# Performance work log

Measured on AMD Instinct MI355X. Metric: run time of the kernel, lower is better.

Reference implementation:

```python
import jax, jax.numpy as jnp
import numpy as np
from jax import lax

B, S, D = 8, 1024, 128

def setup_inputs() -> dict:
    key = jax.random.key(0)
    ks = jax.random.split(key, 6)
    scale = 1.0 / np.sqrt(D)
    return {
        "x": jax.random.normal(ks[0], (B, S, D), dtype=jnp.float32),
        "Wk": jax.random.normal(ks[1], (D, D), dtype=jnp.float32) * scale,
        "Wv": jax.random.normal(ks[2], (D, D), dtype=jnp.float32) * scale,
        "Wq": jax.random.normal(ks[3], (D, D), dtype=jnp.float32) * scale,
        "Wg": jax.random.normal(ks[4], (D, 3), dtype=jnp.float32) * scale,
        "bg": jnp.zeros((3,), dtype=jnp.float32),
    }

def reference(x, Wk, Wv, Wq, Wg, bg):
    b, s, d = x.shape
    k = x @ Wk  # [b,s,d]
    v = x @ Wv
    q = x @ Wq
    gates = jax.nn.sigmoid(x @ Wg + bg)  # [b,s,3]
    alpha, eta, theta = gates[..., 0], gates[..., 1], gates[..., 2]  # [b,s]

    M0 = jnp.zeros((b, d, d), dtype=x.dtype)
    S0 = jnp.zeros((b, d, d), dtype=x.dtype)

    # time-major scan inputs
    xs = (jnp.swapaxes(k, 0, 1), jnp.swapaxes(v, 0, 1), jnp.swapaxes(q, 0, 1),
          jnp.swapaxes(alpha, 0, 1), jnp.swapaxes(eta, 0, 1), jnp.swapaxes(theta, 0, 1))

    def scan_fn(carry, inp):
        M_prev, S_prev = carry
        kt, vt, qt, at, et, tt = inp  # kt/vt/qt: [b,d]; at/et/tt: [b]
        # NOTE: original einsum 'bd,bdd->bd' takes the DIAGONAL of M (faithful)
        diagM = jnp.einsum('bdd->bd', M_prev)  # [b,d]
        yt = qt * diagM
        pred = kt * diagM
        error = pred - vt
        grad = kt[:, :, None] * error[:, None, :]  # outer product [b,d,d]
        S_new = et[:, None, None] * S_prev - tt[:, None, None] * grad
        M_new = (1.0 - at[:, None, None]) * M_prev + S_new
        return (M_new, S_new), yt

    (M_final, S_final), outputs = lax.scan(scan_fn, (M0, S0), xs)
    outputs = jnp.swapaxes(outputs, 0, 1)  # [b,s,d]
    return (outputs, (M_final, S_final))
```

## Files before the change

### kernel.cpp

```cpp
#include <hip/hip_runtime.h>
#include <math.h>

#define NB 8
#define NS 1024
#define ND 128
#define NC 64
#define NL 16

#define OFF_K  0u
#define OFF_Q  1048576u
#define OFF_V  2097152u
#define OFF_E  3145728u
#define OFF_GA 4194304u
#define OFF_GE 4202496u
#define OFF_GT 4210688u
#define OFF_W  4218880u
#define OFF_C  4227072u
#define OFF_P  4235264u

#define PL_A00 (OFF_P)
#define PL_A01 (OFF_P +  65536u)
#define PL_A10 (OFF_P + 131072u)
#define PL_A11 (OFF_P + 196608u)
#define PL_B0  (OFF_P + 262144u)
#define PL_B1  (OFF_P + 327680u)
#define PL_MST (OFF_P + 393216u)
#define PL_SST (OFF_P + 458752u)
#define PL_WCA (OFF_P + 524288u)
#define PL_WCB (OFF_P + 524800u)
#define PL_WCD (OFF_P + 525312u)
#define PL_WRQ (OFF_P + 525824u)
#define PL_WRP (OFF_P + 526336u)
#define PL_WRA (OFF_P + 526848u)
#define OFF_WT (OFF_P + 532480u)
#define WT_LO  49152u

typedef short bf16x8 __attribute__((ext_vector_type(8)));
typedef float f32x4  __attribute__((ext_vector_type(4)));

static __device__ __forceinline__ unsigned short f2bf(float f) {
    unsigned u = __builtin_bit_cast(unsigned, f);
    unsigned r = (u + 0x7FFFu + ((u >> 16) & 1u)) >> 16;
    return (unsigned short)r;
}
static __device__ __forceinline__ float bf2f(unsigned short h) {
    unsigned u = ((unsigned)h) << 16;
    return __builtin_bit_cast(float, u);
}
static __device__ __forceinline__ unsigned pack2(float a, float b) {
    return (unsigned)f2bf(a) | ((unsigned)f2bf(b) << 16);
}
static __device__ __forceinline__ void split2(float a, float b,
                                              unsigned& hi, unsigned& lo) {
    unsigned short ah = f2bf(a), bh = f2bf(b);
    float ar = a - bf2f(ah), br = b - bf2f(bh);
    hi = (unsigned)ah | ((unsigned)bh << 16);
    lo = (unsigned)f2bf(ar) | ((unsigned)f2bf(br) << 16);
}

__global__ __launch_bounds__(256) void wtprep_kernel(
    const float* __restrict__ Wk, const float* __restrict__ Wv,
    const float* __restrict__ Wq, unsigned short* __restrict__ wtg)
{
    const int m    = blockIdx.x >> 4;
    const int cgrp = blockIdx.x & 15;
    const int tid  = threadIdx.x;
    const int cl   = tid >> 5;
    const int h    = tid & 31;
    const int c    = cgrp * 8 + cl;
    const float* W = (m == 0) ? Wk : (m == 1) ? Wv : Wq;

    float f[4];
#pragma unroll
    for (int i = 0; i < 4; ++i)
        f[i] = W[(h * 4 + i) * ND + c];
    uint2 hi, lo;
    split2(f[0], f[1], hi.x, lo.x);
    split2(f[2], f[3], hi.y, lo.y);
    const unsigned base = (unsigned)m * 16384u + (unsigned)c * 128u + (unsigned)h * 4u;
    *(uint2*)&wtg[base]         = hi;
    *(uint2*)&wtg[WT_LO + base] = lo;
}

__global__ __launch_bounds__(256) void proj_mfma(
    const float* __restrict__ x, const unsigned short* __restrict__ wtg,
    const float* __restrict__ Wg, const float* __restrict__ bg,
    float* __restrict__ Kb, float* __restrict__ Vb, float* __restrict__ Qb,
    float* __restrict__ ga, float* __restrict__ ge, float* __restrict__ gt)
{
    __shared__ unsigned short xs_hi[32 * 136];
    __shared__ unsigned short xs_lo[32 * 136];
    __shared__ unsigned short wt_hi[64 * 136];
    __shared__ unsigned short wt_lo[64 * 136];

    const int tid  = threadIdx.x;
    const int bid  = blockIdx.x;
    const int m    = bid >> 9;
    const int rt   = (bid >> 1) & 255;
    const int ch   = bid & 1;
    const int row0 = rt * 32;

    const float4* x4 = (const float4*)x;
#pragma unroll
    for (int l = 0; l < 4; ++l) {
        int idx = tid + l * 256;
        int r = idx >> 5, kq = idx & 31;
        float4 f = x4[(row0 + r) * 32 + kq];
        uint2 hi, lo;
        split2(f.x, f.y, hi.x, lo.x);
        split2(f.z, f.w, hi.y, lo.y);
        *(uint2*)&xs_hi[r * 136 + kq * 4] = hi;
        *(uint2*)&xs_lo[r * 136 + kq * 4] = lo;
    }
    const uint4* wh4 = (const uint4*)(wtg + m * 16384 + ch * 64 * 128);
    const uint4* wl4 = (const uint4*)(wtg + WT_LO + m * 16384 + ch * 64 * 128);
#pragma unroll
    for (int l = 0; l < 4; ++l) {
        int idx = tid + l * 256;
        int c = idx >> 4, u = idx & 15;
        *(uint4*)&wt_hi[c * 136 + u * 8] = wh4[c * 16 + u];
        *(uint4*)&wt_lo[c * 136 + u * 8] = wl4[c * 16 + u];
    }
    __syncthreads();

    const int wid  = tid >> 6;
    const int lane = tid & 63;
    const int rg   = wid >> 1;
    const int cg   = wid & 1;
    const int lrow = rg * 16 + (lane & 15);
    const int quad = lane >> 4;

    f32x4 acc[2];
    acc[0] = (f32x4){0.f, 0.f, 0.f, 0.f};
    acc[1] = (f32x4){0.f, 0.f, 0.f, 0.f};

#pragma unroll
    for (int kk = 0; kk < 4; ++kk) {
        bf16x8 ah = *(const bf16x8*)&xs_hi[lrow * 136 + kk * 32 + quad * 8];
        bf16x8 al = *(const bf16x8*)&xs_lo[lrow * 136 + kk * 32 + quad * 8];
#pragma unroll
        for (int ct = 0; ct < 2; ++ct) {
            int cl = cg * 32 + ct * 16 + (lane & 15);
            bf16x8 bh = *(const bf16x8*)&wt_hi[cl * 136 + kk * 32 + quad * 8];
            bf16x8 bl = *(const bf16x8*)&wt_lo[cl * 136 + kk * 32 + quad * 8];
            acc[ct] = __builtin_amdgcn_mfma_f32_16x16x32_bf16(ah, bh, acc[ct], 0, 0, 0);
            acc[ct] = __builtin_amdgcn_mfma_f32_16x16x32_bf16(ah, bl, acc[ct], 0, 0, 0);
            acc[ct] = __builtin_amdgcn_mfma_f32_16x16x32_bf16(al, bh, acc[ct], 0, 0, 0);
        }
    }

    float* dst = (m == 0) ? Kb : (m == 1) ? Vb : Qb;
#pragma unroll
    for (int ct = 0; ct < 2; ++ct) {
        int ocol = ch * 64 + cg * 32 + ct * 16 + (lane & 15);
#pragma unroll
        for (int r4 = 0; r4 < 4; ++r4) {
            int orow = row0 + rg * 16 + quad * 4 + r4;
            dst[orow * ND + ocol] = acc[ct][r4];
        }
    }

    if (m == 0 && ch == 0 && tid < 96) {
        int r = tid / 3, j = tid % 3;
        float z = bg[j];
        const float* xr = x + (row0 + r) * ND;
#pragma unroll 4
        for (int i = 0; i < ND; ++i)
            z = fmaf(xr[i], Wg[i * 3 + j], z);
        float gate = 1.0f / (1.0f + expf(-z));
        int row = row0 + r;
        float* gd = (j == 0) ? ga : (j == 1) ? ge : gt;
        gd[row] = gate;
    }
}

__global__ __launch_bounds__(128) void scan_phase1(
    const float* __restrict__ Kb, const float* __restrict__ Vb,
    const float* __restrict__ ga, const float* __restrict__ ge,
    const float* __restrict__ gt, float* __restrict__ ws)
{
    __shared__ float la[NL], le[NL], lt[NL];
    const int tid = threadIdx.x;
    const int b   = blockIdx.x >> 6;
    const int c   = blockIdx.x & 63;
    const int t0  = c * NL;
    const int g0  = b * NS + t0;

    if (tid < 16)       la[tid]      = ga[g0 + tid];
    else if (tid < 32)  le[tid - 16] = ge[g0 + tid - 16];
    else if (tid < 48)  lt[tid - 32] = gt[g0 + tid - 32];
    __syncthreads();

    const int d = tid;
    float A00 = 1.f, A01 = 0.f, A10 = 0.f, A11 = 1.f, B0 = 0.f, B1 = 0.f;
    int base = g0 * ND + d;
#pragma unroll
    for (int t = 0; t < NL; ++t) {
        float k = Kb[base], v = Vb[base];
        float a = la[t], e = le[t], th = lt[t];
        float tk = th * k;
        float gg = -tk * k;
        float h  = tk * v;
        float p  = (1.0f - a) + gg;
        float u0 = e * A10;
        float u1 = e * A11;
        float u2 = fmaf(e, B1, h);
        float n00 = fmaf(p, A00, u0), n10 = fmaf(gg, A00, u0);
        float n01 = fmaf(p, A01, u1), n11 = fmaf(gg, A01, u1);
        float nb0 = fmaf(p, B0, u2),  nb1 = fmaf(gg, B0, u2);
        A00 = n00; A01 = n01; A10 = n10; A11 = n11; B0 = nb0; B1 = nb1;
        base += ND;
    }
    const int pidx = (b * NC + c) * ND + d;
    ws[PL_A00 + pidx] = A00;
    ws[PL_A01 + pidx] = A01;
    ws[PL_A10 + pidx] = A10;
    ws[PL_A11 + pidx] = A11;
    ws[PL_B0  + pidx] = B0;
    ws[PL_B1  + pidx] = B1;

    if (tid == 0) {
        float al = 1.f, be = 1.f, de = 0.f;
#pragma unroll
        for (int t = NL - 1; t >= 0; --t) {
            float e1 = le[t];
            float o1 = 1.0f - la[t];
            de = fmaf(e1, de, o1 * be);
            al *= e1;
            be *= o1;
        }
        ws[PL_WCA + b * NC + c] = al;
        ws[PL_WCB + b * NC + c] = be;
        ws[PL_WCD + b * NC + c] = de;
    }
}

__global__ __launch_bounds__(64) void scan_phase2(float* __restrict__ ws)
{
    const int tid = threadIdx.x;
    if (blockIdx.x < 16) {
        const int b = blockIdx.x >> 1;
        const int d = (blockIdx.x & 1) * 64 + tid;
        float m = 0.f, s = 0.f;
        int idx = (b * NC) * ND + d;
#pragma unroll 4
        for (int c = 0; c < NC; ++c) {
            ws[PL_MST + idx] = m;
            ws[PL_SST + idx] = s;
            float A00 = ws[PL_A00 + idx], A01 = ws[PL_A01 + idx];
            float A10 = ws[PL_A10 + idx], A11 = ws[PL_A11 + idx];
            float B0  = ws[PL_B0  + idx], B1  = ws[PL_B1  + idx];
            float nm = fmaf(A00, m, fmaf(A01, s, B0));
            float ns = fmaf(A10, m, fmaf(A11, s, B1));
            m = nm; s = ns;
            idx += ND;
        }
    } else if (tid < 8) {
        const int b = tid;
        float Qp = 1.f, P = 1.f, A = 1.f;
        for (int c = NC - 1; c >= 0; --c) {
            ws[PL_WRQ + b * NC + c] = Qp;
            ws[PL_WRP + b * NC + c] = P;
            ws[PL_WRA + b * NC + c] = A;
            float al = ws[PL_WCA + b * NC + c];
            float be = ws[PL_WCB + b * NC + c];
            float de = ws[PL_WCD + b * NC + c];
            float nA = fmaf(al, A, de * P);
            Qp *= al; P *= be; A = nA;
        }
    }
}

__global__ __launch_bounds__(128) void scan_phase3(
    const float* __restrict__ Kb, const float* __restrict__ Vb,
    const float* __restrict__ Qb,
    const float* __restrict__ ga, const float* __restrict__ ge,
    const float* __restrict__ gt,
    float* __restrict__ out, float* __restrict__ errb,
    float* __restrict__ wb,  float* __restrict__ cb,
    float* __restrict__ ws)
{
    __shared__ float la[NL], le[NL], lt[NL];
    const int tid = threadIdx.x;
    const int b   = blockIdx.x >> 6;
    const int c   = blockIdx.x & 63;
    const int t0  = c * NL;
    const int g0  = b * NS + t0;

    if (tid < 16)       la[tid]      = ga[g0 + tid];
    else if (tid < 32)  le[tid - 16] = ge[g0 + tid - 16];
    else if (tid < 48)  lt[tid - 32] = gt[g0 + tid - 32];
    __syncthreads();

    const int d = tid;
    const int pidx = (b * NC + c) * ND + d;
    float m = ws[PL_MST + pidx];
    float s = ws[PL_SST + pidx];
    int base = g0 * ND + d;
#pragma unroll
    for (int t = 0; t < NL; ++t) {
        float k = Kb[base], v = Vb[base], q = Qb[base];
        float a = la[t], e = le[t], th = lt[t];
        float err = fmaf(k, m, -v);
        out[base]  = q * m;
        errb[base] = err;
        float tk = th * k;
        float u  = fmaf(-(tk * k), m, tk * v);
        s = fmaf(e, s, u);
        m = fmaf(1.0f - a, m, s);
        base += ND;
    }

    if (tid == 0) {
        float Qp = ws[PL_WRQ + b * NC + c];
        float P  = ws[PL_WRP + b * NC + c];
        float A  = ws[PL_WRA + b * NC + c];
#pragma unroll
        for (int t = NL - 1; t >= 0; --t) {
            wb[g0 + t] = -lt[t] * Qp;
            cb[g0 + t] = -lt[t] * A;
            float e1 = le[t];
            float o1 = 1.0f - la[t];
            Qp *= e1;
            P  *= o1;
            A   = fmaf(e1, A, P);
        }
    }
}

__global__ __launch_bounds__(256) void finalgemm_kernel(
    const float* __restrict__ Kb, const float* __restrict__ errb,
    const float* __restrict__ wb, const float* __restrict__ cb,
    float* __restrict__ part)
{
    __shared__ float ks[256 * 16];
    __shared__ float wcs[256 * 2];
    const int tid = threadIdx.x;
    const int bid = blockIdx.x;
    const int b   = bid >> 5;
    const int tc  = (bid >> 3) & 3;
    const int rg  = bid & 7;
    const int bt0 = b * NS + tc * 256;

#pragma unroll
    for (int l = 0; l < 16; ++l) {
        int idx = tid + l * 256;
        int tl = idx >> 4, r = idx & 15;
        ks[tl * 16 + r] = Kb[(bt0 + tl) * ND + rg * 16 + r];
    }
    wcs[tid * 2]     = wb[bt0 + tid];
    wcs[tid * 2 + 1] = cb[bt0 + tid];
    __syncthreads();

    const int j = tid & 127;
    const int h = tid >> 7;
    float accM[8], accS[8];
#pragma unroll
    for (int i = 0; i < 8; ++i) { accM[i] = 0.f; accS[i] = 0.f; }

    int ebase = bt0 * ND + j;
#pragma unroll 2
    for (int t = 0; t < 256; ++t) {
        float ej = errb[ebase];
        float2 wc = *(const float2*)&wcs[t * 2];
        float wej = wc.x * ej, cej = wc.y * ej;
        float4 k0 = *(const float4*)&ks[t * 16 + h * 8];
        float4 k1 = *(const float4*)&ks[t * 16 + h * 8 + 4];
        accS[0] = fmaf(k0.x, wej, accS[0]); accM[0] = fmaf(k0.x, cej, accM[0]);
        accS[1] = fmaf(k0.y, wej, accS[1]); accM[1] = fmaf(k0.y, cej, accM[1]);
        accS[2] = fmaf(k0.z, wej, accS[2]); accM[2] = fmaf(k0.z, cej, accM[2]);
        accS[3] = fmaf(k0.w, wej, accS[3]); accM[3] = fmaf(k0.w, cej, accM[3]);
        accS[4] = fmaf(k1.x, wej, accS[4]); accM[4] = fmaf(k1.x, cej, accM[4]);
        accS[5] = fmaf(k1.y, wej, accS[5]); accM[5] = fmaf(k1.y, cej, accM[5]);
        accS[6] = fmaf(k1.z, wej, accS[6]); accM[6] = fmaf(k1.z, cej, accM[6]);
        accS[7] = fmaf(k1.w, wej, accS[7]); accM[7] = fmaf(k1.w, cej, accM[7]);
        ebase += ND;
    }

    const int robase = rg * 16 + h * 8;
    const unsigned pb = (unsigned)tc * 262144u;
#pragma unroll
    for (int i = 0; i < 8; ++i) {
        int off = b * (ND * ND) + (robase + i) * ND + j;
        part[pb + off]           = accM[i];
        part[pb + 131072u + off] = accS[i];
    }
}

__global__ __launch_bounds__(256) void reduce_kernel(
    const float* __restrict__ part, float* __restrict__ outMS)
{
    int idx = blockIdx.x * 256 + threadIdx.x;
    const float4* p = (const float4*)part;
    float4 a = p[idx];
    float4 b = p[idx + 65536];
    float4 c = p[idx + 131072];
    float4 d = p[idx + 196608];
    float4 r;
    r.x = a.x + b.x + c.x + d.x;
    r.y = a.y + b.y + c.y + d.y;
    r.z = a.z + b.z + c.z + d.z;
    r.w = a.w + b.w + c.w + d.w;
    ((float4*)outMS)[idx] = r;
}

extern "C" void kernel_launch(void* const* d_in, const int* in_sizes, int n_in,
                              void* d_out, int out_size, void* d_ws, size_t ws_size,
                              hipStream_t stream) {
    const float* x  = (const float*)d_in[0];
    const float* Wk = (const float*)d_in[1];
    const float* Wv = (const float*)d_in[2];
    const float* Wq = (const float*)d_in[3];
    const float* Wg = (const float*)d_in[4];
    const float* bg = (const float*)d_in[5];
    float* out = (float*)d_out;
    float* ws  = (float*)d_ws;

    float* Kb  = ws + OFF_K;
    float* Qb  = ws + OFF_Q;
    float* Vb  = ws + OFF_V;
    float* Eb  = ws + OFF_E;
    float* ga  = ws + OFF_GA;
    float* ge  = ws + OFF_GE;
    float* gt  = ws + OFF_GT;
    float* wbf = ws + OFF_W;
    float* cbf = ws + OFF_C;
    float* Pb  = ws + OFF_P;
    unsigned short* wtg = (unsigned short*)(ws + OFF_WT);

    wtprep_kernel<<<48, 256, 0, stream>>>(Wk, Wv, Wq, wtg);
    proj_mfma<<<1536, 256, 0, stream>>>(x, wtg, Wg, bg,
                                        Kb, Vb, Qb, ga, ge, gt);
    scan_phase1<<<NB * NC, 128, 0, stream>>>(Kb, Vb, ga, ge, gt, ws);
    scan_phase2<<<17, 64, 0, stream>>>(ws);
    scan_phase3<<<NB * NC, 128, 0, stream>>>(Kb, Vb, Qb, ga, ge, gt,
                                             out, Eb, wbf, cbf, ws);
    finalgemm_kernel<<<256, 256, 0, stream>>>(Kb, Eb, wbf, cbf, Pb);
    reduce_kernel<<<256, 256, 0, stream>>>(Pb, out + 1048576u);
}
```

Before: 139.1 us.

## Split final GEMM over 16 time chunks and reduce with atomics

The final outer-product accumulation now runs on 1024 blocks of 64 timesteps each instead of 256 blocks of 256, and the separate reduce kernel is gone. Each block adds its partial M and S directly into the output with float atomicAdd, after a memset zeroes that region. This adds parallelism and drops one launch plus the partials round-trip through memory. The cost is sixteen atomic adds per output element and a summation order that is no longer deterministic.

```diff
diff --git a/kernel.cpp b/kernel.cpp
--- a/kernel.cpp
+++ b/kernel.cpp
@@ -46,9 +46,6 @@
 static __device__ __forceinline__ float bf2f(unsigned short h) {
     unsigned u = ((unsigned)h) << 16;
     return __builtin_bit_cast(float, u);
-}
-static __device__ __forceinline__ unsigned pack2(float a, float b) {
-    return (unsigned)f2bf(a) | ((unsigned)f2bf(b) << 16);
 }
 static __device__ __forceinline__ void split2(float a, float b,
                                               unsigned& hi, unsigned& lo) {
@@ -331,25 +328,26 @@
 __global__ __launch_bounds__(256) void finalgemm_kernel(
     const float* __restrict__ Kb, const float* __restrict__ errb,
     const float* __restrict__ wb, const float* __restrict__ cb,
-    float* __restrict__ part)
-{
-    __shared__ float ks[256 * 16];
-    __shared__ float wcs[256 * 2];
+    float* __restrict__ outMS)
+{
+    __shared__ float ks[64 * 16];
+    __shared__ float wcs[64 * 2];
     const int tid = threadIdx.x;
     const int bid = blockIdx.x;
-    const int b   = bid >> 5;
-    const int tc  = (bid >> 3) & 3;
+    const int b   = bid >> 7;
+    const int tc  = (bid >> 3) & 15;
     const int rg  = bid & 7;
-    const int bt0 = b * NS + tc * 256;
-
-#pragma unroll
-    for (int l = 0; l < 16; ++l) {
-        int idx = tid + l * 256;
-        int tl = idx >> 4, r = idx & 15;
-        ks[tl * 16 + r] = Kb[(bt0 + tl) * ND + rg * 16 + r];
-    }
-    wcs[tid * 2]     = wb[bt0 + tid];
-    wcs[tid * 2 + 1] = cb[bt0 + tid];
+    const int bt0 = b * NS + tc * 64;
+
+    {
+        int tl = tid >> 2, r4 = tid & 3;
+        *(float4*)&ks[tl * 16 + r4 * 4] =
+            *(const float4*)&Kb[(bt0 + tl) * ND + rg * 16 + r4 * 4];
+    }
+    if (tid < 64) {
+        wcs[tid * 2]     = wb[bt0 + tid];
+        wcs[tid * 2 + 1] = cb[bt0 + tid];
+    }
     __syncthreads();
 
     const int j = tid & 127;
@@ -359,8 +357,8 @@
     for (int i = 0; i < 8; ++i) { accM[i] = 0.f; accS[i] = 0.f; }
 
     int ebase = bt0 * ND + j;
-#pragma unroll 2
-    for (int t = 0; t < 256; ++t) {
+#pragma unroll 4
+    for (int t = 0; t < 64; ++t) {
         float ej = errb[ebase];
         float2 wc = *(const float2*)&wcs[t * 2];
         float wej = wc.x * ej, cej = wc.y * ej;
@@ -378,30 +376,12 @@
     }
 
     const int robase = rg * 16 + h * 8;
-    const unsigned pb = (unsigned)tc * 262144u;
 #pragma unroll
     for (int i = 0; i < 8; ++i) {
         int off = b * (ND * ND) + (robase + i) * ND + j;
-        part[pb + off]           = accM[i];
-        part[pb + 131072u + off] = accS[i];
-    }
-}
-
-__global__ __launch_bounds__(256) void reduce_kernel(
-    const float* __restrict__ part, float* __restrict__ outMS)
-{
-    int idx = blockIdx.x * 256 + threadIdx.x;
-    const float4* p = (const float4*)part;
-    float4 a = p[idx];
-    float4 b = p[idx + 65536];
-    float4 c = p[idx + 131072];
-    float4 d = p[idx + 196608];
-    float4 r;
-    r.x = a.x + b.x + c.x + d.x;
-    r.y = a.y + b.y + c.y + d.y;
-    r.z = a.z + b.z + c.z + d.z;
-    r.w = a.w + b.w + c.w + d.w;
-    ((float4*)outMS)[idx] = r;
+        atomicAdd(&outMS[off], accM[i]);
+        atomicAdd(&outMS[131072u + off], accS[i]);
+    }
 }
 
 extern "C" void kernel_launch(void* const* d_in, const int* in_sizes, int n_in,
@@ -425,8 +405,9 @@
     float* gt  = ws + OFF_GT;
     float* wbf = ws + OFF_W;
     float* cbf = ws + OFF_C;
-    float* Pb  = ws + OFF_P;
     unsigned short* wtg = (unsigned short*)(ws + OFF_WT);
+
+    hipMemsetAsync(out + 1048576u, 0, 262144u * sizeof(float), stream);
 
     wtprep_kernel<<<48, 256, 0, stream>>>(Wk, Wv, Wq, wtg);
     proj_mfma<<<1536, 256, 0, stream>>>(x, wtg, Wg, bg,
@@ -435,6 +416,6 @@
     scan_phase2<<<17, 64, 0, stream>>>(ws);
     scan_phase3<<<NB * NC, 128, 0, stream>>>(Kb, Vb, Qb, ga, ge, gt,
                                              out, Eb, wbf, cbf, ws);
-    finalgemm_kernel<<<256, 256, 0, stream>>>(Kb, Eb, wbf, cbf, Pb);
-    reduce_kernel<<<256, 256, 0, stream>>>(Pb, out + 1048576u);
-}
+    finalgemm_kernel<<<1024, 256, 0, stream>>>(Kb, Eb, wbf, cbf,
+                                               out + 1048576u);
+}
```

New measurement: 119.0 us. 14.5% less time.
